# Kernel optimization log

Measured on AMD Instinct MI355X. Metric: run time of the kernel, lower is better.

Reference implementation:

```python
import jax, jax.numpy as jnp
import numpy as np

T, B, D = 2048, 16, 1024


def setup_inputs() -> dict:
    key = jax.random.key(0)
    ks = jax.random.split(key, 8)
    std = 1.0 / D ** 0.5
    x = jax.random.normal(ks[0], (T, B, D), dtype=jnp.float32)
    h0 = jnp.zeros((B, D), dtype=jnp.float32)
    Wx = jax.random.uniform(ks[1], (D, D), jnp.float32, -std, std)
    R = jax.random.uniform(ks[2], (D, D), jnp.float32, -std, std)
    bias = jnp.zeros((D,), dtype=jnp.float32)
    W_delta = jax.random.uniform(ks[3], (D, D), jnp.float32, -std * 0.1, std * 0.1)
    b_delta = jnp.full((D,), 3.0, dtype=jnp.float32)  # delta_init
    A = jax.random.uniform(ks[4], (D,), jnp.float32, -0.5, 0.5)  # A_init_range
    W_gate_x = jax.random.uniform(ks[5], (D, D), jnp.float32, -std, std)
    W_gate_h = jax.random.uniform(ks[6], (D, D), jnp.float32, -std, std)
    b_gate = jnp.zeros((D,), dtype=jnp.float32)
    return {"x": x, "h0": h0, "Wx": Wx, "R": R, "bias": bias,
            "W_delta": W_delta, "b_delta": b_delta, "A": A,
            "W_gate_x": W_gate_x, "W_gate_h": W_gate_h, "b_gate": b_gate}


def reference(x, h0, Wx, R, bias, W_delta, b_delta, A, W_gate_x, W_gate_h, b_gate):
    # Input-dependent timestep: dt = softplus(x @ W_delta^T + b_delta), [T,B,D]
    dt = jax.nn.softplus(jnp.einsum('tbd,ed->tbe', x, W_delta) + b_delta)
    # Mamba-style log parameterization: decay_rate in (0,1), alpha in (0,1)
    decay_rate = jnp.exp(-jnp.exp(A))                 # [D]
    alpha = jnp.exp(-dt * decay_rate)                 # [T,B,D]
    # Precompute input projection once (big GEMM outside the scan)
    wx = jnp.einsum('tbd,ed->tbe', x, Wx) + bias      # [T,B,D]

    def step(h, inp):
        wx_t, a_t = inp                               # [B,D], [B,D]
        cand = jnp.tanh(h @ R.T + wx_t)               # nonlinear candidate
        h_new = a_t * h + (1.0 - a_t) * cand          # exponential blend
        return h_new, h_new

    _, h_out = jax.lax.scan(step, h0, (wx, alpha))    # h_out: [T,B,D] == h[1:]

    # h+x selective output gate
    gate_raw = (jnp.einsum('tbd,ed->tbe', x, W_gate_x)
                + jnp.einsum('tbd,ed->tbe', h_out, W_gate_h) + b_gate)
    return h_out * jax.nn.silu(gate_raw)
```

## Files before the change

kernel.cpp:

```cpp
#include <hip/hip_runtime.h>
#include <cstdint>
#include <cstddef>

typedef _Float16 f16;
typedef _Float16 f16x8 __attribute__((ext_vector_type(8)));
typedef _Float16 f16x4v __attribute__((ext_vector_type(4)));
typedef float f32x4 __attribute__((ext_vector_type(4)));
typedef unsigned uint2v __attribute__((ext_vector_type(2)));

#define TT 2048
#define BB 16
#define DD 1024
#define MM (TT*BB)
#define LDST 40
#define FPAD 16

__global__ void cvt_kernel(const float* __restrict__ in, f16* __restrict__ out, int n4){
  int stride = gridDim.x * blockDim.x;
  for (int j = blockIdx.x*blockDim.x + threadIdx.x; j < n4; j += stride){
    float4 v = ((const float4*)in)[j];
    f16x4v o;
    o[0]=(f16)v.x; o[1]=(f16)v.y; o[2]=(f16)v.z; o[3]=(f16)v.w;
    ((f16x4v*)out)[j] = o;
  }
}

__global__ void cvt5_kernel(const float* __restrict__ a0, const float* __restrict__ a1,
                            const float* __restrict__ a2, const float* __restrict__ a3,
                            const float* __restrict__ a4,
                            f16* __restrict__ o0, f16* __restrict__ o1,
                            f16* __restrict__ o2, f16* __restrict__ o3, f16* __restrict__ o4){
  const float* src[5] = {a0,a1,a2,a3,a4};
  f16* dst[5] = {o0,o1,o2,o3,o4};
  int which = blockIdx.y;
  const float* in = src[which];
  f16* out = dst[which];
  int j = blockIdx.x*blockDim.x + threadIdx.x;
  float4 v = ((const float4*)in)[j];
  f16x4v o;
  o[0]=(f16)v.x; o[1]=(f16)v.y; o[2]=(f16)v.z; o[3]=(f16)v.w;
  ((f16x4v*)out)[j] = o;
}

__global__ void init_rec_kernel(const float* __restrict__ h0, f16* __restrict__ hbuf,
                                unsigned* __restrict__ flags){
  int tid = blockIdx.x*blockDim.x + threadIdx.x;
  if (tid < 64*FPAD) flags[tid] = 0u;
  if (tid < BB*DD) hbuf[tid] = (f16)h0[tid];
}

#define GEMM_PROLOGUE() \
  __shared__ f16 As[128*LDST]; \
  __shared__ f16 Bs[128*LDST]; \
  int tid = threadIdx.x; \
  int l = tid & 63, w = tid >> 6; \
  int wr = w >> 1, wc = w & 1; \
  f32x4 acc[4][4]; \
  _Pragma("unroll") for (int i=0;i<4;++i) _Pragma("unroll") for (int jj=0;jj<4;++jj) \
    acc[i][jj] = (f32x4){0.f,0.f,0.f,0.f}; \
  const int r0 = tid >> 2; \
  const int q  = tid & 3;

#define GEMM_KSTEP(Asrc, Bsrc, ktl) { \
  __syncthreads(); \
  _Pragma("unroll") for (int hh=0; hh<2; ++hh){ \
    int row = hh*64 + r0; \
    uint4 va = *(const uint4*)((Asrc) + (size_t)(bm*128+row)*DD + (ktl)*32 + q*8); \
    uint4 vb = *(const uint4*)((Bsrc) + (size_t)(bcol*128+row)*DD + (ktl)*32 + q*8); \
    *(uint4*)(As + row*LDST + q*8) = va; \
    *(uint4*)(Bs + row*LDST + q*8) = vb; \
  } \
  __syncthreads(); \
  int lr = l & 15, kg = (l >> 4) * 8; \
  f16x8 af[4], bf[4]; \
  _Pragma("unroll") for (int i=0;i<4;++i){ \
    af[i] = *(const f16x8*)(As + (wr*64 + i*16 + lr)*LDST + kg); \
    bf[i] = *(const f16x8*)(Bs + (wc*64 + i*16 + lr)*LDST + kg); \
  } \
  _Pragma("unroll") for (int i=0;i<4;++i) \
    _Pragma("unroll") for (int jj=0;jj<4;++jj) \
      acc[i][jj] = __builtin_amdgcn_mfma_f32_16x16x32_f16(af[i], bf[jj], acc[i][jj], 0,0,0); \
}

__global__ __launch_bounds__(256)
void gemm_wa_kernel(const f16* __restrict__ x16,
                    const f16* __restrict__ Wx16, const f16* __restrict__ Wd16,
                    f16* __restrict__ wxo, f16* __restrict__ alo,
                    const float* __restrict__ bias, const float* __restrict__ bd,
                    const float* __restrict__ Aar)
{
  int bm = blockIdx.x, bn = blockIdx.y;
  int alpha_path = (bn >= 8);
  int bcol = bn & 7;
  const f16* Bw = alpha_path ? Wd16 : Wx16;

  GEMM_PROLOGUE();
  for (int kt = 0; kt < 32; ++kt) GEMM_KSTEP(x16, Bw, kt);

  int lr = l & 15, lh = l >> 4;
  #pragma unroll
  for (int i=0;i<4;++i){
    #pragma unroll
    for (int jj=0;jj<4;++jj){
      #pragma unroll
      for (int r=0;r<4;++r){
        int row = bm*128 + wr*64 + i*16 + lh*4 + r;
        int col = bcol*128 + wc*64 + jj*16 + lr;
        float v = acc[i][jj][r];
        size_t off = (size_t)row*DD + col;
        if (!alpha_path){
          wxo[off] = (f16)(v + bias[col]);
        } else {
          float pre = v + bd[col];
          float sp  = (pre > 20.f) ? pre : log1pf(expf(pre));
          float decay = expf(-expf(Aar[col]));
          alo[off] = (f16)expf(-sp*decay);
        }
      }
    }
  }
}

__global__ __launch_bounds__(256)
void gemm_fin_kernel(const f16* __restrict__ hout16, const f16* __restrict__ x16,
                     const f16* __restrict__ Wgh16, const f16* __restrict__ Wgx16,
                     float* __restrict__ out, const float* __restrict__ bg)
{
  int bm = blockIdx.x, bcol = blockIdx.y;

  GEMM_PROLOGUE();
  for (int kt = 0; kt < 32; ++kt) GEMM_KSTEP(hout16, Wgh16, kt);
  for (int kt = 0; kt < 32; ++kt) GEMM_KSTEP(x16,    Wgx16, kt);

  int lr = l & 15, lh = l >> 4;
  #pragma unroll
  for (int i=0;i<4;++i){
    #pragma unroll
    for (int jj=0;jj<4;++jj){
      #pragma unroll
      for (int r=0;r<4;++r){
        int row = bm*128 + wr*64 + i*16 + lh*4 + r;
        int col = bcol*128 + wc*64 + jj*16 + lr;
        float g = acc[i][jj][r] + bg[col];
        size_t off = (size_t)row*DD + col;
        float hval = (float)hout16[off];
        out[off] = hval * g / (1.f + expf(-g));
      }
    }
  }
}

__global__ __launch_bounds__(64)
void rec_kernel(const f16* __restrict__ Rf, const f16* __restrict__ wx,
                const f16* __restrict__ alpha, const float* __restrict__ h0,
                f16* __restrict__ hbuf, f16* __restrict__ hout,
                unsigned* __restrict__ flags)
{
  __shared__ f16 Rlds[32*64*8];

  int l = threadIdx.x;
  int j = blockIdx.x;
  int e0 = j * 16;

  #pragma unroll
  for (int kt=0; kt<32; ++kt){
    int e = e0 + (l & 15);
    int d = kt*32 + (l >> 4)*8;
    *(uint4*)(Rlds + ((size_t)kt*64 + l)*8) = *(const uint4*)(Rf + (size_t)e*DD + d);
  }

  int b = l & 15, rr0 = (l >> 4) * 4;
  float4 hstate = *(const float4*)(h0 + (size_t)b*DD + e0 + rr0);
  __syncthreads();

  f32x4 wxv, alv;
  {
    f16x4v wh = *(const f16x4v*)(wx + (size_t)b*DD + e0 + rr0);
    f16x4v ah = *(const f16x4v*)(alpha + (size_t)b*DD + e0 + rr0);
    #pragma unroll
    for (int r=0;r<4;++r){ wxv[r] = (float)wh[r]; alv[r] = (float)ah[r]; }
  }

  for (int t = 0; t < TT; ++t){
    if (t > 0){
      const unsigned* fp = flags + l*FPAD;
      int guard = 0;
      unsigned long long notready = 1ull;
      while (notready && guard < 2000000){
        unsigned fv = __hip_atomic_load(fp, __ATOMIC_RELAXED, __HIP_MEMORY_SCOPE_AGENT);
        notready = __ballot(fv < (unsigned)t);
        ++guard;
        if (notready) __builtin_amdgcn_s_sleep(1);
      }
    }

    const f16* hb = hbuf + (size_t)(t & 1) * (BB*DD);
    f16x8 hfr[32];
    #pragma unroll
    for (int kt=0; kt<32; ++kt){
      const f16* hp = hb + (size_t)b*DD + kt*32 + (l >> 4)*8;
      asm volatile("global_load_dwordx4 %0, %1, off sc0 sc1"
                   : "=v"(hfr[kt]) : "v"(hp) : "memory");
    }

    f32x4 accv[4];
    #pragma unroll
    for (int c=0;c<4;++c) accv[c] = (f32x4){0.f,0.f,0.f,0.f};

    asm volatile("s_waitcnt vmcnt(24)" ::: "memory");
    __builtin_amdgcn_sched_barrier(0);
    #pragma unroll
    for (int kt=0; kt<8; ++kt){
      f16x8 a = *(const f16x8*)(Rlds + ((size_t)kt*64 + l)*8);
      accv[kt&3] = __builtin_amdgcn_mfma_f32_16x16x32_f16(a, hfr[kt], accv[kt&3], 0, 0, 0);
    }
    asm volatile("s_waitcnt vmcnt(16)" ::: "memory");
    __builtin_amdgcn_sched_barrier(0);
    #pragma unroll
    for (int kt=8; kt<16; ++kt){
      f16x8 a = *(const f16x8*)(Rlds + ((size_t)kt*64 + l)*8);
      accv[kt&3] = __builtin_amdgcn_mfma_f32_16x16x32_f16(a, hfr[kt], accv[kt&3], 0, 0, 0);
    }
    asm volatile("s_waitcnt vmcnt(8)" ::: "memory");
    __builtin_amdgcn_sched_barrier(0);

    int tn = (t+1 < TT) ? (t+1) : t;
    size_t offn = ((size_t)tn*BB + b)*DD + e0 + rr0;
    f16x4v whn = *(const f16x4v*)(wx + offn);
    f16x4v ahn = *(const f16x4v*)(alpha + offn);

    #pragma unroll
    for (int kt=16; kt<24; ++kt){
      f16x8 a = *(const f16x8*)(Rlds + ((size_t)kt*64 + l)*8);
      accv[kt&3] = __builtin_amdgcn_mfma_f32_16x16x32_f16(a, hfr[kt], accv[kt&3], 0, 0, 0);
    }
    asm volatile("s_waitcnt vmcnt(0)" ::: "memory");
    __builtin_amdgcn_sched_barrier(0);
    #pragma unroll
    for (int kt=24; kt<32; ++kt){
      f16x8 a = *(const f16x8*)(Rlds + ((size_t)kt*64 + l)*8);
      accv[kt&3] = __builtin_amdgcn_mfma_f32_16x16x32_f16(a, hfr[kt], accv[kt&3], 0, 0, 0);
    }
    f32x4 acc = (accv[0]+accv[1]) + (accv[2]+accv[3]);

    f16x4v h4;
    float hs[4] = {hstate.x, hstate.y, hstate.z, hstate.w};
    #pragma unroll
    for (int r=0;r<4;++r){
      float z = acc[r] + wxv[r];
      float cand = tanhf(z);
      float hn = alv[r]*hs[r] + (1.f - alv[r])*cand;
      hs[r] = hn;
      h4[r] = (f16)hn;
    }
    hstate = (float4){hs[0], hs[1], hs[2], hs[3]};

    f16* hw = hbuf + (size_t)((t+1) & 1) * (BB*DD) + (size_t)b*DD + e0 + rr0;
    uint2v hv = __builtin_bit_cast(uint2v, h4);
    asm volatile("global_store_dwordx2 %0, %1, off sc0 sc1"
                 :: "v"(hw), "v"(hv) : "memory");
    asm volatile("s_waitcnt vmcnt(0)" ::: "memory");
    if (l == 0)
      __hip_atomic_store(flags + j*FPAD, (unsigned)(t+1),
                         __ATOMIC_RELAXED, __HIP_MEMORY_SCOPE_AGENT);

    *(f16x4v*)(hout + ((size_t)t*BB + b)*DD + e0 + rr0) = h4;
    #pragma unroll
    for (int r=0;r<4;++r){ wxv[r] = (float)whn[r]; alv[r] = (float)ahn[r]; }
  }
}

extern "C" void kernel_launch(void* const* d_in, const int* in_sizes, int n_in,
                              void* d_out, int out_size, void* d_ws, size_t ws_size,
                              hipStream_t stream)
{
  const float* x    = (const float*)d_in[0];
  const float* h0   = (const float*)d_in[1];
  const float* Wx   = (const float*)d_in[2];
  const float* R    = (const float*)d_in[3];
  const float* bias = (const float*)d_in[4];
  const float* Wd   = (const float*)d_in[5];
  const float* bd   = (const float*)d_in[6];
  const float* Aar  = (const float*)d_in[7];
  const float* Wgx  = (const float*)d_in[8];
  const float* Wgh  = (const float*)d_in[9];
  const float* bg   = (const float*)d_in[10];
  float* out = (float*)d_out;

  char* ws = (char*)d_ws;
  size_t off = 0;
  auto carve = [&](size_t bytes) -> void* {
    void* p = ws + off;
    off += (bytes + 255) & ~(size_t)255;
    return p;
  };
  f16* x16    = (f16*)carve((size_t)MM*DD*2);
  f16* Wx16   = (f16*)carve((size_t)DD*DD*2);
  f16* Wd16   = (f16*)carve((size_t)DD*DD*2);
  f16* Wgx16  = (f16*)carve((size_t)DD*DD*2);
  f16* Wgh16  = (f16*)carve((size_t)DD*DD*2);
  f16* R16    = (f16*)carve((size_t)DD*DD*2);
  f16* wx16   = (f16*)carve((size_t)MM*DD*2);
  f16* al16   = (f16*)carve((size_t)MM*DD*2);
  f16* hout16 = (f16*)carve((size_t)MM*DD*2);
  f16* hbuf   = (f16*)carve((size_t)2*BB*DD*2);
  unsigned* flags = (unsigned*)carve(64*FPAD*4);
  if (off > ws_size) return;

  cvt_kernel<<<1024, 256, 0, stream>>>(x, x16, MM*DD/4);
  dim3 g5(DD*DD/4/256, 5);
  cvt5_kernel<<<g5, 256, 0, stream>>>(Wx, Wd, Wgx, Wgh, R,
                                      Wx16, Wd16, Wgx16, Wgh16, R16);
  init_rec_kernel<<<64, 256, 0, stream>>>(h0, hbuf, flags);

  dim3 gwa(MM/128, 16);
  gemm_wa_kernel<<<gwa, 256, 0, stream>>>(x16, Wx16, Wd16, wx16, al16, bias, bd, Aar);

  rec_kernel<<<64, 64, 0, stream>>>(R16, wx16, al16, h0, hbuf, hout16, flags);

  dim3 gfin(MM/128, DD/128);
  gemm_fin_kernel<<<gfin, 256, 0, stream>>>(hout16, x16, Wgh16, Wgx16, out, bg);
}
```

Measured before the change: 7.092 ms.

## Load GEMM tiles directly into LDS with XOR swizzle; spin before sleeping

The GEMM k-step now uses global_load_lds to copy global tiles straight into shared memory. This skips the register round-trip, and an XOR-swizzled unpadded layout replaces the padded LDST stride to avoid bank conflicts. Separately, the recurrent kernel's flag wait now busy-polls for the first 16 iterations before issuing s_sleep, to cut wake-up latency on the serial per-timestep chain. The swizzle has to match exactly between the write and read sides, and the extra spinning adds memory traffic.

After: 7.009 ms. No clear change (-1.2%).

```diff
diff --git a/kernel.cpp b/kernel.cpp
--- a/kernel.cpp
+++ b/kernel.cpp
@@ -12,7 +12,6 @@
 #define BB 16
 #define DD 1024
 #define MM (TT*BB)
-#define LDST 40
 #define FPAD 16
 
 __global__ void cvt_kernel(const float* __restrict__ in, f16* __restrict__ out, int n4){
@@ -50,32 +49,35 @@
 }
 
 #define GEMM_PROLOGUE() \
-  __shared__ f16 As[128*LDST]; \
-  __shared__ f16 Bs[128*LDST]; \
+  __shared__ f16 As[128*32]; \
+  __shared__ f16 Bs[128*32]; \
   int tid = threadIdx.x; \
   int l = tid & 63, w = tid >> 6; \
   int wr = w >> 1, wc = w & 1; \
   f32x4 acc[4][4]; \
   _Pragma("unroll") for (int i=0;i<4;++i) _Pragma("unroll") for (int jj=0;jj<4;++jj) \
-    acc[i][jj] = (f32x4){0.f,0.f,0.f,0.f}; \
-  const int r0 = tid >> 2; \
-  const int q  = tid & 3;
+    acc[i][jj] = (f32x4){0.f,0.f,0.f,0.f};
 
 #define GEMM_KSTEP(Asrc, Bsrc, ktl) { \
   __syncthreads(); \
   _Pragma("unroll") for (int hh=0; hh<2; ++hh){ \
-    int row = hh*64 + r0; \
-    uint4 va = *(const uint4*)((Asrc) + (size_t)(bm*128+row)*DD + (ktl)*32 + q*8); \
-    uint4 vb = *(const uint4*)((Bsrc) + (size_t)(bcol*128+row)*DD + (ktl)*32 + q*8); \
-    *(uint4*)(As + row*LDST + q*8) = va; \
-    *(uint4*)(Bs + row*LDST + q*8) = vb; \
+    int r = hh*64 + (tid>>2); \
+    int q = (tid&3) ^ (r&3); \
+    const f16* ga = (Asrc) + (size_t)(bm*128+r)*DD + (ktl)*32 + q*8; \
+    const f16* gb = (Bsrc) + (size_t)(bcol*128+r)*DD + (ktl)*32 + q*8; \
+    __builtin_amdgcn_global_load_lds((__attribute__((address_space(1))) void*)ga, \
+        (__attribute__((address_space(3))) void*)(As + hh*2048 + tid*8), 16, 0, 0); \
+    __builtin_amdgcn_global_load_lds((__attribute__((address_space(1))) void*)gb, \
+        (__attribute__((address_space(3))) void*)(Bs + hh*2048 + tid*8), 16, 0, 0); \
   } \
   __syncthreads(); \
-  int lr = l & 15, kg = (l >> 4) * 8; \
+  int lr = l & 15, g = l >> 4; \
   f16x8 af[4], bf[4]; \
   _Pragma("unroll") for (int i=0;i<4;++i){ \
-    af[i] = *(const f16x8*)(As + (wr*64 + i*16 + lr)*LDST + kg); \
-    bf[i] = *(const f16x8*)(Bs + (wc*64 + i*16 + lr)*LDST + kg); \
+    int Ra = wr*64 + i*16 + lr; \
+    int Rb = wc*64 + i*16 + lr; \
+    af[i] = *(const f16x8*)(As + Ra*32 + ((g ^ (Ra & 3)) * 8)); \
+    bf[i] = *(const f16x8*)(Bs + Rb*32 + ((g ^ (Rb & 3)) * 8)); \
   } \
   _Pragma("unroll") for (int i=0;i<4;++i) \
     _Pragma("unroll") for (int jj=0;jj<4;++jj) \
@@ -190,7 +192,7 @@
         unsigned fv = __hip_atomic_load(fp, __ATOMIC_RELAXED, __HIP_MEMORY_SCOPE_AGENT);
         notready = __ballot(fv < (unsigned)t);
         ++guard;
-        if (notready) __builtin_amdgcn_s_sleep(1);
+        if (notready && guard > 16) __builtin_amdgcn_s_sleep(1);
       }
     }
 
```
